# Kernel tuning notes

Hardware: AMD Instinct MI355X
Metric: run time of the kernel (lower is better)

The kernel has to match this reference:

```python
import jax, jax.numpy as jnp
import numpy as np

QMAX = 127.0  # int8 symmetric

def fake_quant(v):
    # symmetric per-tensor int8 quant -> dequant
    s = jnp.maximum(jnp.max(jnp.abs(v)), 1e-8) / QMAX
    return jnp.round(jnp.clip(v / s, -QMAX, QMAX)) * s

def setup_inputs() -> dict:
    key = jax.random.key(0)
    k1, k2, k3 = jax.random.split(key, 3)
    B, C, H, W = 64, 3, 224, 224
    D, P = 768, 8
    x = jax.random.normal(k1, (B, C, H, W), dtype=jnp.float32)
    w = jax.random.normal(k2, (D, C, P, P), dtype=jnp.float32) * 0.02
    b = jax.random.normal(k3, (D,), dtype=jnp.float32) * 0.02
    return {"x": x, "w": w, "b": b}

def reference(x, w, b):
    B, C, H, W = x.shape
    D, _, P, _ = w.shape
    gh, gw = H // P, W // P
    # quantized conv (HMQConv2d): fake-quant activations and weights, then patchify GEMM
    xq = fake_quant(x)
    wq = fake_quant(w)
    # extract non-overlapping PxP patches: [B, C, gh, P, gw, P]
    xp = xq.reshape(B, C, gh, P, gw, P)
    # conv stride=kernel=P  ==  patch matmul: out [B, gh, gw, D]
    out = jnp.einsum('bchpwq,dchq->bhwd', xp.transpose(0, 1, 2, 3, 4, 5), wq,
                     optimize=True) if False else jnp.einsum('bcxpyq,dcpq->bxyd', xp, wq)
    out = out + b
    # flatten(2).transpose(1,2): [B, N, D]
    out = out.reshape(B, gh * gw, D)
    # norm is Identity (norm_layer=None)
    return out
```

## Files before the change

### kernel.cpp

```cpp
#include <hip/hip_runtime.h>
#include <stdint.h>


using f32x4 = __attribute__((ext_vector_type(4))) float;
using i32x4 = __attribute__((ext_vector_type(4))) int;

static __device__ __forceinline__ uint32_t q4i8(float4 v, float inv_s) {
  uint32_t r;
  int q0 = (int)rintf(fminf(fmaxf(v.x * inv_s, -127.0f), 127.0f));
  int q1 = (int)rintf(fminf(fmaxf(v.y * inv_s, -127.0f), 127.0f));
  int q2 = (int)rintf(fminf(fmaxf(v.z * inv_s, -127.0f), 127.0f));
  int q3 = (int)rintf(fminf(fmaxf(v.w * inv_s, -127.0f), 127.0f));
  r = (uint32_t)(q0 & 0xff) | ((uint32_t)(q1 & 0xff) << 8) |
      ((uint32_t)(q2 & 0xff) << 16) | ((uint32_t)(q3 & 0xff) << 24);
  return r;
}

#define NBX 1024
#define NBW 64
__global__ void absmax_k(const float4* __restrict__ x, int nx4,
                         const float4* __restrict__ w, int nw4,
                         float* __restrict__ partials) {
  __shared__ float red[4];
  float m = 0.0f;
  if (blockIdx.x < NBX) {
    for (int i = blockIdx.x * 256 + threadIdx.x; i < nx4; i += NBX * 256) {
      float4 u = x[i];
      m = fmaxf(m, fabsf(u.x)); m = fmaxf(m, fabsf(u.y));
      m = fmaxf(m, fabsf(u.z)); m = fmaxf(m, fabsf(u.w));
    }
  } else {
    for (int i = (blockIdx.x - NBX) * 256 + threadIdx.x; i < nw4; i += NBW * 256) {
      float4 u = w[i];
      m = fmaxf(m, fabsf(u.x)); m = fmaxf(m, fabsf(u.y));
      m = fmaxf(m, fabsf(u.z)); m = fmaxf(m, fabsf(u.w));
    }
  }
#pragma unroll
  for (int off = 32; off > 0; off >>= 1) m = fmaxf(m, __shfl_down(m, off, 64));
  if ((threadIdx.x & 63) == 0) red[threadIdx.x >> 6] = m;
  __syncthreads();
  if (threadIdx.x == 0) {
    m = fmaxf(fmaxf(red[0], red[1]), fmaxf(red[2], red[3]));
    partials[blockIdx.x] = m;
  }
}

#define NQXB 1792
#define NQWB 36
__global__ __launch_bounds__(256) void quant_xw_k(
    const float* __restrict__ x, const float4* __restrict__ w4,
    uint4* __restrict__ Aq, uint4* __restrict__ Wq,
    const float* __restrict__ partials, float* __restrict__ slots) {
  __shared__ float redx[4];
  __shared__ float redw_s;
  __shared__ uint2 stg8[28][26];
  const int tid = threadIdx.x;

  float mx = 0.0f;
  for (int i = tid; i < NBX; i += 256) mx = fmaxf(mx, partials[i]);
#pragma unroll
  for (int off = 32; off > 0; off >>= 1) mx = fmaxf(mx, __shfl_down(mx, off, 64));
  if ((tid & 63) == 0) redx[tid >> 6] = mx;
  if (tid < 64) {
    float mw = partials[NBX + tid];
#pragma unroll
    for (int off = 32; off > 0; off >>= 1) mw = fmaxf(mw, __shfl_down(mw, off, 64));
    if (tid == 0) redw_s = mw;
  }
  __syncthreads();
  float sx = fmaxf(fmaxf(redx[0], redx[1]), fmaxf(redx[2], redx[3]));
  sx = fmaxf(sx, 1e-8f) * (1.0f / 127.0f);
  float sw = fmaxf(redw_s, 1e-8f) * (1.0f / 127.0f);
  if (blockIdx.x == 0 && tid == 0) { slots[0] = sx; slots[1] = sw; }

  if (blockIdx.x < NQXB) {
    const float inv = 1.0f / sx;
    const int b  = blockIdx.x / 28;
    const int gx = blockIdx.x - b * 28;
    for (int t = tid; t < 672; t += 256) {
      const int r  = t / 28;
      const int gy = t - r * 28;
      const int c = r >> 3, p = r & 7;
      const float4* src =
          (const float4*)(x + (size_t)((b * 3 + c) * 224 + gx * 8 + p) * 224);
      float4 a0 = src[gy * 2], a1 = src[gy * 2 + 1];
      uint2 q;
      q.x = q4i8(a0, inv);
      q.y = q4i8(a1, inv);
      stg8[gy][r] = q;
    }
    __syncthreads();
    uint4* dst = Aq + (size_t)(b * 784 + gx * 28) * 12;
    for (int t = tid; t < 336; t += 256) {
      const int gy = t / 12;
      const int j  = t - gy * 12;
      uint2 lo = stg8[gy][2 * j], hi = stg8[gy][2 * j + 1];
      uint4 v; v.x = lo.x; v.y = lo.y; v.z = hi.x; v.w = hi.y;
      dst[t] = v;
    }
  } else {
    const float inv = 1.0f / sw;
    const int g = (blockIdx.x - NQXB) * 256 + tid;
    float4 a0 = w4[g * 4], a1 = w4[g * 4 + 1];
    float4 a2 = w4[g * 4 + 2], a3 = w4[g * 4 + 3];
    uint4 q;
    q.x = q4i8(a0, inv); q.y = q4i8(a1, inv);
    q.z = q4i8(a2, inv); q.w = q4i8(a3, inv);
    Wq[g] = q;
  }
}

__global__ __launch_bounds__(256) void gemm_k(
    const uint4* __restrict__ Aq, const uint4* __restrict__ Wq,
    const float* __restrict__ bias, const float* __restrict__ slots,
    float* __restrict__ out) {
  __shared__ float tr[4 * 1280];
  const int tid  = threadIdx.x;
  const int lane = tid & 63;
  const int wid  = tid >> 6;
  const int wm   = wid >> 1;
  const int wn   = wid & 1;
  const int lm   = lane & 15;
  const int lq   = lane >> 4;
  const int m0   = blockIdx.x * 128;
  const int n0   = blockIdx.y * 128;

  int abase[4], bbase[4];
#pragma unroll
  for (int tm = 0; tm < 4; ++tm)
    abase[tm] = (m0 + wm * 64 + tm * 16 + lm) * 12 + lq;
#pragma unroll
  for (int tn = 0; tn < 4; ++tn)
    bbase[tn] = (n0 + wn * 64 + tn * 16 + lm) * 12 + lq;

  i32x4 acc[4][4] = {};

#pragma unroll
  for (int ks = 0; ks < 3; ++ks) {
    i32x4 af[4], bf[4];
#pragma unroll
    for (int tm = 0; tm < 4; ++tm)
      af[tm] = __builtin_bit_cast(i32x4, Aq[abase[tm] + ks * 4]);
#pragma unroll
    for (int tn = 0; tn < 4; ++tn)
      bf[tn] = __builtin_bit_cast(i32x4, Wq[bbase[tn] + ks * 4]);
#pragma unroll
    for (int tm = 0; tm < 4; ++tm)
#pragma unroll
      for (int tn = 0; tn < 4; ++tn)
        acc[tm][tn] = __builtin_amdgcn_mfma_i32_16x16x64_i8(
            af[tm], bf[tn], acc[tm][tn], 0, 0, 0);
  }

  const float scale = slots[0] * slots[1];
  float* T = &tr[wid * 1280];
  const int c4 = lane & 15;
  const int gc = n0 + wn * 64 + c4 * 4;
  const float4 bv = *(const float4*)&bias[gc];

#pragma unroll
  for (int tm = 0; tm < 4; ++tm) {
#pragma unroll
    for (int tn = 0; tn < 4; ++tn) {
      f32x4 f;
#pragma unroll
      for (int j = 0; j < 4; ++j) f[j] = (float)acc[tm][tn][j];
      *(f32x4*)&T[(tn * 16 + lm) * 20 + lq * 4] = f;
    }
    asm volatile("s_waitcnt lgkmcnt(0)" ::: "memory");
#pragma unroll
    for (int i = 0; i < 4; ++i) {
      const int s = (lane >> 4) + i * 4;
      float4 v;
      v.x = T[(c4 * 4 + 0) * 20 + s];
      v.y = T[(c4 * 4 + 1) * 20 + s];
      v.z = T[(c4 * 4 + 2) * 20 + s];
      v.w = T[(c4 * 4 + 3) * 20 + s];
      float4 o;
      o.x = fmaf(v.x, scale, bv.x);
      o.y = fmaf(v.y, scale, bv.y);
      o.z = fmaf(v.z, scale, bv.z);
      o.w = fmaf(v.w, scale, bv.w);
      const int gm = m0 + wm * 64 + tm * 16 + s;
      *(float4*)&out[(size_t)gm * 768 + gc] = o;
    }
    asm volatile("s_waitcnt lgkmcnt(0)" ::: "memory");
  }
}


extern "C" void kernel_launch(void* const* d_in, const int* in_sizes, int n_in,
                              void* d_out, int out_size, void* d_ws, size_t ws_size,
                              hipStream_t stream) {
  const float* xf = (const float*)d_in[0];
  const float4* x4 = (const float4*)d_in[0];
  const float4* w4 = (const float4*)d_in[1];
  const float* bias = (const float*)d_in[2];
  float* out = (float*)d_out;

  char* ws = (char*)d_ws;
  float* slots    = (float*)ws;
  float* partials = (float*)(ws + 256);
  uint4* Wq       = (uint4*)(ws + 8192);
  uint4* Aq       = (uint4*)(ws + 8192 + 147456);

  const int nx4 = 9633792 / 4;
  const int nw4 = 147456 / 4;

  absmax_k<<<NBX + NBW, 256, 0, stream>>>(x4, nx4, w4, nw4, partials);
  quant_xw_k<<<NQXB + NQWB, 256, 0, stream>>>(xf, w4, Aq, Wq, partials, slots);
  gemm_k<<<dim3(392, 6), 256, 0, stream>>>(Aq, Wq, bias, slots, out);
}
```

Baseline: 200.3 us.

## Fuse absmax and quantization into one kernel using an atomic grid barrier

Removes the separate absmax pass over x and w. Each block now loads its slice into registers, reduces a local absmax, publishes it with an atomic max, and spins on a counter until every block has arrived. It then quantizes from the registers it already holds. This cuts one full read of the input and one kernel launch, at the cost of a tiny init kernel and a grid-wide spin barrier. That barrier can deadlock if the 1828 blocks of 256 threads cannot all be resident at once, which is why __launch_bounds__(256,8) is set.

After: 420.1 us. +109.7%, slower.

```diff
diff --git a/kernel.cpp b/kernel.cpp
--- a/kernel.cpp
+++ b/kernel.cpp
@@ -6,89 +6,86 @@
 using i32x4 = __attribute__((ext_vector_type(4))) int;
 
 static __device__ __forceinline__ uint32_t q4i8(float4 v, float inv_s) {
-  uint32_t r;
   int q0 = (int)rintf(fminf(fmaxf(v.x * inv_s, -127.0f), 127.0f));
   int q1 = (int)rintf(fminf(fmaxf(v.y * inv_s, -127.0f), 127.0f));
   int q2 = (int)rintf(fminf(fmaxf(v.z * inv_s, -127.0f), 127.0f));
   int q3 = (int)rintf(fminf(fmaxf(v.w * inv_s, -127.0f), 127.0f));
-  r = (uint32_t)(q0 & 0xff) | ((uint32_t)(q1 & 0xff) << 8) |
-      ((uint32_t)(q2 & 0xff) << 16) | ((uint32_t)(q3 & 0xff) << 24);
-  return r;
-}
-
-#define NBX 1024
-#define NBW 64
-__global__ void absmax_k(const float4* __restrict__ x, int nx4,
-                         const float4* __restrict__ w, int nw4,
-                         float* __restrict__ partials) {
-  __shared__ float red[4];
-  float m = 0.0f;
-  if (blockIdx.x < NBX) {
-    for (int i = blockIdx.x * 256 + threadIdx.x; i < nx4; i += NBX * 256) {
-      float4 u = x[i];
-      m = fmaxf(m, fabsf(u.x)); m = fmaxf(m, fabsf(u.y));
-      m = fmaxf(m, fabsf(u.z)); m = fmaxf(m, fabsf(u.w));
-    }
-  } else {
-    for (int i = (blockIdx.x - NBX) * 256 + threadIdx.x; i < nw4; i += NBW * 256) {
-      float4 u = w[i];
-      m = fmaxf(m, fabsf(u.x)); m = fmaxf(m, fabsf(u.y));
-      m = fmaxf(m, fabsf(u.z)); m = fmaxf(m, fabsf(u.w));
-    }
-  }
-#pragma unroll
-  for (int off = 32; off > 0; off >>= 1) m = fmaxf(m, __shfl_down(m, off, 64));
-  if ((threadIdx.x & 63) == 0) red[threadIdx.x >> 6] = m;
-  __syncthreads();
-  if (threadIdx.x == 0) {
-    m = fmaxf(fmaxf(red[0], red[1]), fmaxf(red[2], red[3]));
-    partials[blockIdx.x] = m;
-  }
-}
-
-#define NQXB 1792
-#define NQWB 36
-__global__ __launch_bounds__(256) void quant_xw_k(
+  return (uint32_t)(q0 & 0xff) | ((uint32_t)(q1 & 0xff) << 8) |
+         ((uint32_t)(q2 & 0xff) << 16) | ((uint32_t)(q3 & 0xff) << 24);
+}
+
+#define NXB 1792
+#define NWB 36
+
+__global__ void init_k(uint32_t* __restrict__ sync) {
+  if (threadIdx.x < 4) sync[threadIdx.x] = 0;
+}
+
+__global__ __launch_bounds__(256, 8) void prep_k(
     const float* __restrict__ x, const float4* __restrict__ w4,
     uint4* __restrict__ Aq, uint4* __restrict__ Wq,
-    const float* __restrict__ partials, float* __restrict__ slots) {
-  __shared__ float redx[4];
-  __shared__ float redw_s;
+    uint32_t* __restrict__ sync, float* __restrict__ slots) {
+  __shared__ float red[4];
+  __shared__ float s_scale;
   __shared__ uint2 stg8[28][26];
   const int tid = threadIdx.x;
-
-  float mx = 0.0f;
-  for (int i = tid; i < NBX; i += 256) mx = fmaxf(mx, partials[i]);
-#pragma unroll
-  for (int off = 32; off > 0; off >>= 1) mx = fmaxf(mx, __shfl_down(mx, off, 64));
-  if ((tid & 63) == 0) redx[tid >> 6] = mx;
-  if (tid < 64) {
-    float mw = partials[NBX + tid];
-#pragma unroll
-    for (int off = 32; off > 0; off >>= 1) mw = fmaxf(mw, __shfl_down(mw, off, 64));
-    if (tid == 0) redw_s = mw;
-  }
-  __syncthreads();
-  float sx = fmaxf(fmaxf(redx[0], redx[1]), fmaxf(redx[2], redx[3]));
-  sx = fmaxf(sx, 1e-8f) * (1.0f / 127.0f);
-  float sw = fmaxf(redw_s, 1e-8f) * (1.0f / 127.0f);
-  if (blockIdx.x == 0 && tid == 0) { slots[0] = sx; slots[1] = sw; }
-
-  if (blockIdx.x < NQXB) {
-    const float inv = 1.0f / sx;
-    const int b  = blockIdx.x / 28;
-    const int gx = blockIdx.x - b * 28;
-    for (int t = tid; t < 672; t += 256) {
-      const int r  = t / 28;
-      const int gy = t - r * 28;
-      const int c = r >> 3, p = r & 7;
-      const float4* src =
-          (const float4*)(x + (size_t)((b * 3 + c) * 224 + gx * 8 + p) * 224);
-      float4 a0 = src[gy * 2], a1 = src[gy * 2 + 1];
-      uint2 q;
-      q.x = q4i8(a0, inv);
-      q.y = q4i8(a1, inv);
-      stg8[gy][r] = q;
+  const int bid = blockIdx.x;
+
+  if (bid < NXB) {
+    const int b  = bid / 28;
+    const int gx = bid - b * 28;
+    float4 A0[3], A1[3];
+    float mx = 0.0f;
+#pragma unroll
+    for (int s = 0; s < 3; ++s) {
+      if (s < 2 || tid < 160) {
+        const int t  = tid + s * 256;
+        const int r  = t / 28;
+        const int gy = t - r * 28;
+        const int c = r >> 3, p = r & 7;
+        const float4* src =
+            (const float4*)(x + (size_t)((b * 3 + c) * 224 + gx * 8 + p) * 224);
+        A0[s] = src[gy * 2];
+        A1[s] = src[gy * 2 + 1];
+        mx = fmaxf(mx, fmaxf(fmaxf(fabsf(A0[s].x), fabsf(A0[s].y)),
+                             fmaxf(fabsf(A0[s].z), fabsf(A0[s].w))));
+        mx = fmaxf(mx, fmaxf(fmaxf(fabsf(A1[s].x), fabsf(A1[s].y)),
+                             fmaxf(fabsf(A1[s].z), fabsf(A1[s].w))));
+      }
+    }
+#pragma unroll
+    for (int off = 32; off > 0; off >>= 1) mx = fmaxf(mx, __shfl_down(mx, off, 64));
+    if ((tid & 63) == 0) red[tid >> 6] = mx;
+    __syncthreads();
+    if (tid == 0) {
+      float m = fmaxf(fmaxf(red[0], red[1]), fmaxf(red[2], red[3]));
+      __hip_atomic_fetch_max(&sync[0], __float_as_uint(m),
+                             __ATOMIC_RELAXED, __HIP_MEMORY_SCOPE_AGENT);
+      __hip_atomic_fetch_add(&sync[1], 1u,
+                             __ATOMIC_RELEASE, __HIP_MEMORY_SCOPE_AGENT);
+      while (__hip_atomic_load(&sync[1], __ATOMIC_ACQUIRE,
+                               __HIP_MEMORY_SCOPE_AGENT) < NXB)
+        __builtin_amdgcn_s_sleep(2);
+      uint32_t mb = __hip_atomic_load(&sync[0], __ATOMIC_RELAXED,
+                                      __HIP_MEMORY_SCOPE_AGENT);
+      s_scale = fmaxf(__uint_as_float(mb), 1e-8f) * (1.0f / 127.0f);
+    }
+    __syncthreads();
+    const float sxs = s_scale;
+    if (bid == 0 && tid == 0) slots[0] = sxs;
+
+    const float inv = 1.0f / sxs;
+#pragma unroll
+    for (int s = 0; s < 3; ++s) {
+      if (s < 2 || tid < 160) {
+        const int t  = tid + s * 256;
+        const int r  = t / 28;
+        const int gy = t - r * 28;
+        uint2 q;
+        q.x = q4i8(A0[s], inv);
+        q.y = q4i8(A1[s], inv);
+        stg8[gy][r] = q;
+      }
     }
     __syncthreads();
     uint4* dst = Aq + (size_t)(b * 784 + gx * 28) * 12;
@@ -100,13 +97,39 @@
       dst[t] = v;
     }
   } else {
-    const float inv = 1.0f / sw;
-    const int g = (blockIdx.x - NQXB) * 256 + tid;
-    float4 a0 = w4[g * 4], a1 = w4[g * 4 + 1];
-    float4 a2 = w4[g * 4 + 2], a3 = w4[g * 4 + 3];
+    const int g = (bid - NXB) * 256 + tid;
+    float4 B0 = w4[g * 4], B1 = w4[g * 4 + 1];
+    float4 B2 = w4[g * 4 + 2], B3 = w4[g * 4 + 3];
+    float mw = 0.0f;
+    mw = fmaxf(mw, fmaxf(fmaxf(fabsf(B0.x), fabsf(B0.y)), fmaxf(fabsf(B0.z), fabsf(B0.w))));
+    mw = fmaxf(mw, fmaxf(fmaxf(fabsf(B1.x), fabsf(B1.y)), fmaxf(fabsf(B1.z), fabsf(B1.w))));
+    mw = fmaxf(mw, fmaxf(fmaxf(fabsf(B2.x), fabsf(B2.y)), fmaxf(fabsf(B2.z), fabsf(B2.w))));
+    mw = fmaxf(mw, fmaxf(fmaxf(fabsf(B3.x), fabsf(B3.y)), fmaxf(fabsf(B3.z), fabsf(B3.w))));
+#pragma unroll
+    for (int off = 32; off > 0; off >>= 1) mw = fmaxf(mw, __shfl_down(mw, off, 64));
+    if ((tid & 63) == 0) red[tid >> 6] = mw;
+    __syncthreads();
+    if (tid == 0) {
+      float m = fmaxf(fmaxf(red[0], red[1]), fmaxf(red[2], red[3]));
+      __hip_atomic_fetch_max(&sync[2], __float_as_uint(m),
+                             __ATOMIC_RELAXED, __HIP_MEMORY_SCOPE_AGENT);
+      __hip_atomic_fetch_add(&sync[3], 1u,
+                             __ATOMIC_RELEASE, __HIP_MEMORY_SCOPE_AGENT);
+      while (__hip_atomic_load(&sync[3], __ATOMIC_ACQUIRE,
+                               __HIP_MEMORY_SCOPE_AGENT) < NWB)
+        __builtin_amdgcn_s_sleep(2);
+      uint32_t mb = __hip_atomic_load(&sync[2], __ATOMIC_RELAXED,
+                                      __HIP_MEMORY_SCOPE_AGENT);
+      s_scale = fmaxf(__uint_as_float(mb), 1e-8f) * (1.0f / 127.0f);
+    }
+    __syncthreads();
+    const float sws = s_scale;
+    if (bid == NXB && tid == 0) slots[1] = sws;
+
+    const float inv = 1.0f / sws;
     uint4 q;
-    q.x = q4i8(a0, inv); q.y = q4i8(a1, inv);
-    q.z = q4i8(a2, inv); q.w = q4i8(a3, inv);
+    q.x = q4i8(B0, inv); q.y = q4i8(B1, inv);
+    q.z = q4i8(B2, inv); q.w = q4i8(B3, inv);
     Wq[g] = q;
   }
 }
@@ -194,21 +217,17 @@
                               void* d_out, int out_size, void* d_ws, size_t ws_size,
                               hipStream_t stream) {
   const float* xf = (const float*)d_in[0];
-  const float4* x4 = (const float4*)d_in[0];
   const float4* w4 = (const float4*)d_in[1];
   const float* bias = (const float*)d_in[2];
   float* out = (float*)d_out;
 
   char* ws = (char*)d_ws;
   float* slots    = (float*)ws;
-  float* partials = (float*)(ws + 256);
+  uint32_t* sync  = (uint32_t*)(ws + 64);
   uint4* Wq       = (uint4*)(ws + 8192);
   uint4* Aq       = (uint4*)(ws + 8192 + 147456);
 
-  const int nx4 = 9633792 / 4;
-  const int nw4 = 147456 / 4;
-
-  absmax_k<<<NBX + NBW, 256, 0, stream>>>(x4, nx4, w4, nw4, partials);
-  quant_xw_k<<<NQXB + NQWB, 256, 0, stream>>>(xf, w4, Aq, Wq, partials, slots);
+  init_k<<<1, 64, 0, stream>>>(sync);
+  prep_k<<<NXB + NWB, 256, 0, stream>>>(xf, w4, Aq, Wq, sync, slots);
   gemm_k<<<dim3(392, 6), 256, 0, stream>>>(Aq, Wq, bias, slots, out);
 }
```
